# Performance work log

Hardware: AMD Instinct MI355X
Metric: run time of the kernel (lower is better)

## Reference

```python
import jax, jax.numpy as jnp
import numpy as np

STYLE_DIM = 512
NUM_DOMAINS = 8
BATCH = 16384
N_DEC_LAYERS = 4
N_EXP_LAYERS = 4   # each expert: Linear+ReLU x3, then Linear


def setup_inputs() -> dict:
    key = jax.random.key(0)
    ks = jax.random.split(key, 6)
    D, E, B = STYLE_DIM, NUM_DOMAINS, BATCH
    scale = 1.0 / np.sqrt(D)  # ~ torch Linear default init scale
    s = jax.random.normal(ks[0], (B, D), dtype=jnp.float32)
    y = jax.random.randint(ks[1], (B,), 0, E, dtype=jnp.int32)
    # decomposer params: stacked [L, out, in] / [L, out]
    dec_W = jax.random.uniform(ks[2], (N_DEC_LAYERS, D, D), jnp.float32, -scale, scale)
    dec_b = jax.random.uniform(ks[3], (N_DEC_LAYERS, D), jnp.float32, -scale, scale)
    # expert params: stacked [E, L, out, in] / [E, L, out]
    exp_W = jax.random.uniform(ks[4], (E, N_EXP_LAYERS, D, D), jnp.float32, -scale, scale)
    exp_b = jax.random.uniform(ks[5], (E, N_EXP_LAYERS, D), jnp.float32, -scale, scale)
    return {"s": s, "y": y, "dec_W": dec_W, "dec_b": dec_b, "exp_W": exp_W, "exp_b": exp_b}


def reference(s, y, dec_W, dec_b, exp_W, exp_b):
    h = s
    for l in range(N_DEC_LAYERS):
        h = jax.nn.relu(jnp.einsum('bi,oi->bo', h, dec_W[l]) + dec_b[l])
    s_unrelated = h                      # [B, D]
    s_related = s - s_unrelated          # [B, D]

    # run ALL experts on every sample (faithful to original dense compute)
    x = jnp.broadcast_to(s_related[:, None, :], (s.shape[0], NUM_DOMAINS, s.shape[1]))
    for l in range(N_EXP_LAYERS):
        x = jnp.einsum('bei,eoi->beo', x, exp_W[:, l]) + exp_b[:, l]
        if l < N_EXP_LAYERS - 1:
            x = jax.nn.relu(x)
    # gather the per-sample domain output: out[idx, y]
    s_related_tilde = jnp.take_along_axis(x, y[:, None, None].astype(jnp.int32), axis=1)[:, 0, :]
    s_tilde = s_related_tilde + s_unrelated
    return s_tilde
```

## Files before the change

kernel.cpp:

```cpp
#include <hip/hip_runtime.h>
#include <stdint.h>

#define BB 16384
#define PR2 16896
#define MAXT2 264

typedef short bf16x8 __attribute__((ext_vector_type(8)));
typedef float f32x4 __attribute__((ext_vector_type(4)));
typedef unsigned short us4v __attribute__((ext_vector_type(4)));

typedef __attribute__((address_space(1))) unsigned short gus_t;
typedef __attribute__((address_space(3))) unsigned short lus_t;

__device__ __forceinline__ unsigned short f2bf(float f) {
    unsigned int u = __float_as_uint(f);
    u += 0x7fffu + ((u >> 16) & 1u);
    return (unsigned short)(u >> 16);
}
__device__ __forceinline__ float bf2f(unsigned short h) {
    return __uint_as_float(((unsigned int)h) << 16);
}

__device__ __forceinline__ void gld16(const unsigned short* g, unsigned short* l) {
    __builtin_amdgcn_global_load_lds(
        reinterpret_cast<const gus_t*>(reinterpret_cast<uintptr_t>(g)),
        reinterpret_cast<lus_t*>(reinterpret_cast<uintptr_t>(l)),
        16, 0, 0);
}

__global__ void cvt_bf16(const float* __restrict__ src, unsigned short* __restrict__ dst, int n4) {
    int stride = gridDim.x * blockDim.x;
    for (int i = blockIdx.x * blockDim.x + threadIdx.x; i < n4; i += stride) {
        f32x4 v = reinterpret_cast<const f32x4*>(src)[i];
        us4v o;
        o[0] = f2bf(v[0]); o[1] = f2bf(v[1]); o[2] = f2bf(v[2]); o[3] = f2bf(v[3]);
        reinterpret_cast<us4v*>(dst)[i] = o;
    }
}

__global__ void bucket_init(int* perm, int* counts, int* cursors, int* tile_exp) {
    int i = blockIdx.x * blockDim.x + threadIdx.x;
    if (i < PR2) perm[i] = -1;
    if (i < 8) { counts[i] = 0; cursors[i] = 0; }
    if (i < MAXT2) tile_exp[i] = 0;
}

__global__ __launch_bounds__(1024) void bucket_count(const int* __restrict__ y, int* counts) {
    __shared__ int lc[8];
    const int t = threadIdx.x;
    if (t < 8) lc[t] = 0;
    __syncthreads();
    atomicAdd(&lc[y[blockIdx.x * 1024 + t]], 1);
    __syncthreads();
    if (t < 8) atomicAdd(&counts[t], lc[t]);
}

__global__ void bucket_scan(const int* __restrict__ counts, int* starts, int* tile_exp) {
    if (threadIdx.x == 0 && blockIdx.x == 0) {
        int s = 0;
        for (int e = 0; e < 8; ++e) {
            starts[e] = s;
            int nt = (counts[e] + 63) >> 6;
            for (int t = 0; t < nt; ++t) tile_exp[(s >> 6) + t] = e;
            s += nt << 6;
        }
        starts[8] = s;
    }
}

__global__ __launch_bounds__(1024) void bucket_scatter(const int* __restrict__ y,
                                                       const int* __restrict__ starts,
                                                       int* cursors, int* perm) {
    __shared__ int lc[8];
    __shared__ int lbase[8];
    const int t = threadIdx.x;
    if (t < 8) lc[t] = 0;
    __syncthreads();
    const int i = blockIdx.x * 1024 + t;
    const int e = y[i];
    const int r = atomicAdd(&lc[e], 1);
    __syncthreads();
    if (t < 8) lbase[t] = atomicAdd(&cursors[t], lc[t]);
    __syncthreads();
    perm[starts[e] + lbase[e] + r] = i;
}

#define STAGEW(s_, b_) do {                                              \
    const unsigned short* wp_ = Wl + ((s_) >> 4) * 262144                \
                              + (((s_) & 15) << 5) + wbase;              \
    unsigned short* ld_ = ls + 32768 + ((b_) << 14) + (t << 3);          \
    gld16(wp_,          ld_);                                            \
    gld16(wp_ +  65536, ld_ +  4096);                                    \
    gld16(wp_ + 131072, ld_ +  8192);                                    \
    gld16(wp_ + 196608, ld_ + 12288);                                    \
} while (0)

template <int PHASE>
__global__ __launch_bounds__(512) void fused4(
    const float* __restrict__ sf32,
    const unsigned short* __restrict__ srelg,
    const unsigned short* __restrict__ Wb,
    const float* __restrict__ biasb,
    unsigned short* __restrict__ srel_out,
    unsigned short* __restrict__ h_out,
    const unsigned short* __restrict__ h_in,
    float* __restrict__ outf,
    const int* __restrict__ perm,
    const int* __restrict__ tile_exp,
    const int* __restrict__ starts8)
{
    __shared__ __align__(16) unsigned short ls[81920];

    const int bid = blockIdx.x;
    int tile;
    if (PHASE == 0) {
        tile = ((bid & 7) << 5) + (bid >> 3);
    } else {
        tile = (bid & 7) * 33 + (bid >> 3);
        if ((tile << 6) >= starts8[0]) return;
    }

    const unsigned short* Wl;
    const float* bl;
    if (PHASE == 0) { Wl = Wb; bl = biasb; }
    else {
        const int e = tile_exp[tile];
        Wl = Wb + ((size_t)e << 20);
        bl = biasb + (e << 11);
    }

    const int t = threadIdx.x;
    const int w = t >> 6;
    const int lane = t & 63;
    const int lr = lane & 15;
    const int kg = lane >> 4;

    const int wbase = ((t >> 2) << 9) + (((t & 3) ^ ((t >> 3) & 3)) << 3);
    const int asrc_c = (t & 56) | ((t ^ (t >> 6)) & 7);
    const int axor = lr & 7;
    int arow_e[4], bvo[4];
#pragma unroll
    for (int m = 0; m < 4; ++m) arow_e[m] = ((m << 4) + lr) << 9;
#pragma unroll
    for (int j = 0; j < 4; ++j)
        bvo[j] = (((w << 6) + (j << 4) + lr) << 5) + ((kg ^ ((lr >> 1) & 3)) << 3);

    float bball[16];
#pragma unroll
    for (int l = 0; l < 4; ++l)
#pragma unroll
        for (int j = 0; j < 4; ++j)
            bball[(l << 2) + j] = bl[(l << 9) + (w << 6) + (j << 4) + lr];
    asm volatile("s_waitcnt vmcnt(0)" ::: "memory");

    if (PHASE == 0) {
#pragma unroll
        for (int c8 = 0; c8 < 8; ++c8) {
            const int grow = (tile << 6) + (c8 << 3) + (t >> 6);
            const float* sp = sf32 + (((size_t)grow) << 9) + (asrc_c << 3);
            f32x4 v0 = *reinterpret_cast<const f32x4*>(sp);
            f32x4 v1 = *reinterpret_cast<const f32x4*>(sp + 4);
            bf16x8 o;
#pragma unroll
            for (int q = 0; q < 4; ++q) { o[q] = (short)f2bf(v0[q]); o[q + 4] = (short)f2bf(v1[q]); }
            *reinterpret_cast<bf16x8*>(&ls[(c8 << 12) + (t << 3)]) = o;
        }
        asm volatile("s_waitcnt lgkmcnt(0)" ::: "memory");
    } else {
#pragma unroll
        for (int c8 = 0; c8 < 8; ++c8) {
            int pr = perm[(tile << 6) + (c8 << 3) + (t >> 6)];
            if (pr < 0) pr = 0;
            gld16(srelg + (((size_t)pr) << 9) + (asrc_c << 3), ls + (c8 << 12) + (t << 3));
        }
    }
    STAGEW(0, 0);
    STAGEW(1, 1);

    f32x4 acc[4][4];
#pragma unroll
    for (int m = 0; m < 4; ++m)
#pragma unroll
        for (int j = 0; j < 4; ++j)
            acc[m][j] = f32x4{0.f, 0.f, 0.f, 0.f};

    int cur = 0;
    for (int s = 0; s < 64; ++s) {
        if (s < 63) asm volatile("s_waitcnt vmcnt(4)" ::: "memory");
        else        asm volatile("s_waitcnt vmcnt(0)" ::: "memory");
        __builtin_amdgcn_s_barrier();
        asm volatile("" ::: "memory");

        int nb = cur + 2; if (nb >= 3) nb -= 3;
        if (s + 2 < 64) STAGEW(s + 2, nb);

        const int st = s & 15;
        const int sb = (st >> 1) << 6;
        const int klo = ((((st & 1) << 2) | kg) ^ axor) << 3;
        const unsigned short* lW = ls + 32768 + (cur << 14);
        bf16x8 af[4], bv[4];
#pragma unroll
        for (int m = 0; m < 4; ++m)
            af[m] = *reinterpret_cast<const bf16x8*>(&ls[arow_e[m] + sb + klo]);
#pragma unroll
        for (int j = 0; j < 4; ++j)
            bv[j] = *reinterpret_cast<const bf16x8*>(&lW[bvo[j]]);
        __builtin_amdgcn_s_setprio(1);
#pragma unroll
        for (int m = 0; m < 4; ++m)
#pragma unroll
            for (int j = 0; j < 4; ++j)
                acc[m][j] = __builtin_amdgcn_mfma_f32_16x16x32_bf16(af[m], bv[j], acc[m][j], 0, 0, 0);
        __builtin_amdgcn_s_setprio(0);

        if (st == 15 && s < 63) {
            asm volatile("" ::: "memory");
            __builtin_amdgcn_s_barrier();
            asm volatile("" ::: "memory");
            const int lbb = (s >> 4) << 2;
#pragma unroll
            for (int m = 0; m < 4; ++m)
#pragma unroll
                for (int j = 0; j < 4; ++j) {
#pragma unroll
                    for (int reg = 0; reg < 4; ++reg) {
                        const int row = (m << 4) + (kg << 2) + reg;
                        const float v = fmaxf(acc[m][j][reg] + bball[lbb + j], 0.f);
                        const int swc = (w << 3) + (((j << 1) + (lr >> 3)) ^ (row & 7));
                        ls[(row << 9) + (swc << 3) + (lr & 7)] = f2bf(v);
                    }
                    acc[m][j] = f32x4{0.f, 0.f, 0.f, 0.f};
                }
            asm volatile("s_waitcnt lgkmcnt(0)" ::: "memory");
            __builtin_amdgcn_s_barrier();
            asm volatile("" ::: "memory");
        }
        cur = cur + 1 < 3 ? cur + 1 : 0;
    }

    if (PHASE == 0) {
        asm volatile("" ::: "memory");
        __syncthreads();
#pragma unroll
        for (int m = 0; m < 4; ++m)
#pragma unroll
            for (int j = 0; j < 4; ++j)
#pragma unroll
                for (int reg = 0; reg < 4; ++reg) {
                    const int row = (m << 4) + (kg << 2) + reg;
                    const int col = (w << 6) + (j << 4) + lr;
                    const float h = fmaxf(acc[m][j][reg] + bball[12 + j], 0.f);
                    const float sv = sf32[(((size_t)((tile << 6) + row)) << 9) + col];
                    const int swc = (w << 3) + (((j << 1) + (lr >> 3)) ^ (row & 7));
                    const int idx = (row << 9) + (swc << 3) + (lr & 7);
                    ls[idx] = f2bf(sv - h);
                    ls[32768 + idx] = f2bf(h);
                }
        __syncthreads();
#pragma unroll
        for (int c8 = 0; c8 < 8; ++c8) {
            const int row = (c8 << 3) + (t >> 6);
            const size_t go = (((size_t)((tile << 6) + row)) << 9) + (asrc_c << 3);
            bf16x8 va = *reinterpret_cast<const bf16x8*>(&ls[(c8 << 12) + (t << 3)]);
            bf16x8 vh = *reinterpret_cast<const bf16x8*>(&ls[32768 + (c8 << 12) + (t << 3)]);
            *reinterpret_cast<bf16x8*>(&srel_out[go]) = va;
            *reinterpret_cast<bf16x8*>(&h_out[go]) = vh;
        }
    } else {
#pragma unroll
        for (int m = 0; m < 4; ++m) {
#pragma unroll
            for (int reg = 0; reg < 4; ++reg) {
                const int row = (m << 4) + (kg << 2) + reg;
                const int pr = perm[(tile << 6) + row];
                if (pr >= 0) {
#pragma unroll
                    for (int j = 0; j < 4; ++j) {
                        const int col = (w << 6) + (j << 4) + lr;
                        const size_t gi = (((size_t)pr) << 9) + col;
                        outf[gi] = acc[m][j][reg] + bball[12 + j] + bf2f(h_in[gi]);
                    }
                }
            }
        }
    }
}

extern "C" void kernel_launch(void* const* d_in, const int* in_sizes, int n_in,
                              void* d_out, int out_size, void* d_ws, size_t ws_size,
                              hipStream_t stream)
{
    const float* s     = (const float*)d_in[0];
    const int*   y     = (const int*)d_in[1];
    const float* dec_W = (const float*)d_in[2];
    const float* dec_b = (const float*)d_in[3];
    const float* exp_W = (const float*)d_in[4];
    const float* exp_b = (const float*)d_in[5];
    float* out = (float*)d_out;

    unsigned short* decWb = (unsigned short*)d_ws;
    unsigned short* expWb = decWb + 4 * 512 * 512;
    unsigned short* srel  = expWb + 8 * 4 * 512 * 512;
    unsigned short* hbuf  = srel + (size_t)BB * 512;
    int* perm     = (int*)(hbuf + (size_t)BB * 512);
    int* counts   = perm + PR2;
    int* cursors  = counts + 8;
    int* starts   = cursors + 8;
    int* tile_exp = starts + 9;

    cvt_bf16<<<256, 256, 0, stream>>>(dec_W, decWb, (4 * 512 * 512) / 4);
    cvt_bf16<<<2048, 256, 0, stream>>>(exp_W, expWb, (8 * 4 * 512 * 512) / 4);

    bucket_init<<<(PR2 + 255) / 256, 256, 0, stream>>>(perm, counts, cursors, tile_exp);
    bucket_count<<<BB / 1024, 1024, 0, stream>>>(y, counts);
    bucket_scan<<<1, 64, 0, stream>>>(counts, starts, tile_exp);
    bucket_scatter<<<BB / 1024, 1024, 0, stream>>>(y, starts, cursors, perm);

    fused4<0><<<256, 512, 0, stream>>>(s, nullptr, decWb, dec_b, srel, hbuf,
                                       nullptr, nullptr, nullptr, nullptr, nullptr);
    fused4<1><<<MAXT2, 512, 0, stream>>>(nullptr, srel, expWb, exp_b, nullptr, nullptr,
                                         hbuf, out, perm, tile_exp, starts + 8);
}
```

Before: 192.0 us.

## Load weight fragments directly from global into registers, shrink LDS for two blocks/CU

Weight tiles are no longer staged through LDS with async global-to-LDS copies and a triple buffer. Each lane now loads its B fragments straight from global memory into registers, using a three-deep register prefetch per layer. LDS drops to the activation tile only (64 KB), and launch bounds request two blocks per CU to raise occupancy. The cost is uncoalesced, per-lane 16-byte weight reads hitting L2, with no cross-wave sharing of weights inside a block, plus extra epilogue passes to write h and s_rel out through the smaller LDS.

```diff
diff --git a/kernel.cpp b/kernel.cpp
--- a/kernel.cpp
+++ b/kernel.cpp
@@ -85,18 +85,8 @@
     perm[starts[e] + lbase[e] + r] = i;
 }
 
-#define STAGEW(s_, b_) do {                                              \
-    const unsigned short* wp_ = Wl + ((s_) >> 4) * 262144                \
-                              + (((s_) & 15) << 5) + wbase;              \
-    unsigned short* ld_ = ls + 32768 + ((b_) << 14) + (t << 3);          \
-    gld16(wp_,          ld_);                                            \
-    gld16(wp_ +  65536, ld_ +  4096);                                    \
-    gld16(wp_ + 131072, ld_ +  8192);                                    \
-    gld16(wp_ + 196608, ld_ + 12288);                                    \
-} while (0)
-
 template <int PHASE>
-__global__ __launch_bounds__(512) void fused4(
+__global__ __launch_bounds__(512, 2) void fused4(
     const float* __restrict__ sf32,
     const unsigned short* __restrict__ srelg,
     const unsigned short* __restrict__ Wb,
@@ -109,7 +99,7 @@
     const int* __restrict__ tile_exp,
     const int* __restrict__ starts8)
 {
-    __shared__ __align__(16) unsigned short ls[81920];
+    __shared__ __align__(16) unsigned short ls[32768];
 
     const int bid = blockIdx.x;
     int tile;
@@ -135,15 +125,16 @@
     const int lr = lane & 15;
     const int kg = lane >> 4;
 
-    const int wbase = ((t >> 2) << 9) + (((t & 3) ^ ((t >> 3) & 3)) << 3);
     const int asrc_c = (t & 56) | ((t ^ (t >> 6)) & 7);
     const int axor = lr & 7;
-    int arow_e[4], bvo[4];
+    int arow_e[4];
 #pragma unroll
     for (int m = 0; m < 4; ++m) arow_e[m] = ((m << 4) + lr) << 9;
+
+    const unsigned short* wp[4];
 #pragma unroll
     for (int j = 0; j < 4; ++j)
-        bvo[j] = (((w << 6) + (j << 4) + lr) << 5) + ((kg ^ ((lr >> 1) & 3)) << 3);
+        wp[j] = Wl + (((size_t)((w << 6) + (j << 4) + lr)) << 9) + (kg << 3);
 
     float bball[16];
 #pragma unroll
@@ -151,7 +142,6 @@
 #pragma unroll
         for (int j = 0; j < 4; ++j)
             bball[(l << 2) + j] = bl[(l << 9) + (w << 6) + (j << 4) + lr];
-    asm volatile("s_waitcnt vmcnt(0)" ::: "memory");
 
     if (PHASE == 0) {
 #pragma unroll
@@ -165,7 +155,6 @@
             for (int q = 0; q < 4; ++q) { o[q] = (short)f2bf(v0[q]); o[q + 4] = (short)f2bf(v1[q]); }
             *reinterpret_cast<bf16x8*>(&ls[(c8 << 12) + (t << 3)]) = o;
         }
-        asm volatile("s_waitcnt lgkmcnt(0)" ::: "memory");
     } else {
 #pragma unroll
         for (int c8 = 0; c8 < 8; ++c8) {
@@ -173,9 +162,9 @@
             if (pr < 0) pr = 0;
             gld16(srelg + (((size_t)pr) << 9) + (asrc_c << 3), ls + (c8 << 12) + (t << 3));
         }
-    }
-    STAGEW(0, 0);
-    STAGEW(1, 1);
+        asm volatile("s_waitcnt vmcnt(0)" ::: "memory");
+    }
+    __syncthreads();
 
     f32x4 acc[4][4];
 #pragma unroll
@@ -184,40 +173,40 @@
         for (int j = 0; j < 4; ++j)
             acc[m][j] = f32x4{0.f, 0.f, 0.f, 0.f};
 
-    int cur = 0;
-    for (int s = 0; s < 64; ++s) {
-        if (s < 63) asm volatile("s_waitcnt vmcnt(4)" ::: "memory");
-        else        asm volatile("s_waitcnt vmcnt(0)" ::: "memory");
-        __builtin_amdgcn_s_barrier();
-        asm volatile("" ::: "memory");
-
-        int nb = cur + 2; if (nb >= 3) nb -= 3;
-        if (s + 2 < 64) STAGEW(s + 2, nb);
-
-        const int st = s & 15;
-        const int sb = (st >> 1) << 6;
-        const int klo = ((((st & 1) << 2) | kg) ^ axor) << 3;
-        const unsigned short* lW = ls + 32768 + (cur << 14);
-        bf16x8 af[4], bv[4];
-#pragma unroll
-        for (int m = 0; m < 4; ++m)
-            af[m] = *reinterpret_cast<const bf16x8*>(&ls[arow_e[m] + sb + klo]);
-#pragma unroll
-        for (int j = 0; j < 4; ++j)
-            bv[j] = *reinterpret_cast<const bf16x8*>(&lW[bvo[j]]);
-        __builtin_amdgcn_s_setprio(1);
-#pragma unroll
-        for (int m = 0; m < 4; ++m)
-#pragma unroll
-            for (int j = 0; j < 4; ++j)
-                acc[m][j] = __builtin_amdgcn_mfma_f32_16x16x32_bf16(af[m], bv[j], acc[m][j], 0, 0, 0);
-        __builtin_amdgcn_s_setprio(0);
-
-        if (st == 15 && s < 63) {
-            asm volatile("" ::: "memory");
-            __builtin_amdgcn_s_barrier();
-            asm volatile("" ::: "memory");
-            const int lbb = (s >> 4) << 2;
+    for (int l = 0; l < 4; ++l) {
+        const size_t lofs = ((size_t)l) << 18;
+
+        bf16x8 bv[3][4];
+#pragma unroll
+        for (int j = 0; j < 4; ++j) bv[0][j] = *reinterpret_cast<const bf16x8*>(wp[j] + lofs);
+#pragma unroll
+        for (int j = 0; j < 4; ++j) bv[1][j] = *reinterpret_cast<const bf16x8*>(wp[j] + lofs + 32);
+
+#pragma unroll
+        for (int st = 0; st < 16; ++st) {
+            const int cur = st % 3;
+            const int nxt = (st + 2) % 3;
+            if (st + 2 < 16) {
+#pragma unroll
+                for (int j = 0; j < 4; ++j)
+                    bv[nxt][j] = *reinterpret_cast<const bf16x8*>(wp[j] + lofs + (st + 2) * 32);
+            }
+            const int sb = (st >> 1) << 6;
+            const int klo = ((((st & 1) << 2) | kg) ^ axor) << 3;
+            bf16x8 af[4];
+#pragma unroll
+            for (int m = 0; m < 4; ++m)
+                af[m] = *reinterpret_cast<const bf16x8*>(&ls[arow_e[m] + sb + klo]);
+#pragma unroll
+            for (int m = 0; m < 4; ++m)
+#pragma unroll
+                for (int j = 0; j < 4; ++j)
+                    acc[m][j] = __builtin_amdgcn_mfma_f32_16x16x32_bf16(af[m], bv[cur][j], acc[m][j], 0, 0, 0);
+        }
+
+        if (l < 3) {
+            __syncthreads();
+            const int lbb = l << 2;
 #pragma unroll
             for (int m = 0; m < 4; ++m)
 #pragma unroll
@@ -231,15 +220,11 @@
                     }
                     acc[m][j] = f32x4{0.f, 0.f, 0.f, 0.f};
                 }
-            asm volatile("s_waitcnt lgkmcnt(0)" ::: "memory");
-            __builtin_amdgcn_s_barrier();
-            asm volatile("" ::: "memory");
-        }
-        cur = cur + 1 < 3 ? cur + 1 : 0;
+            __syncthreads();
+        }
     }
 
     if (PHASE == 0) {
-        asm volatile("" ::: "memory");
         __syncthreads();
 #pragma unroll
         for (int m = 0; m < 4; ++m)
@@ -252,19 +237,35 @@
                     const float h = fmaxf(acc[m][j][reg] + bball[12 + j], 0.f);
                     const float sv = sf32[(((size_t)((tile << 6) + row)) << 9) + col];
                     const int swc = (w << 3) + (((j << 1) + (lr >> 3)) ^ (row & 7));
-                    const int idx = (row << 9) + (swc << 3) + (lr & 7);
-                    ls[idx] = f2bf(sv - h);
-                    ls[32768 + idx] = f2bf(h);
+                    ls[(row << 9) + (swc << 3) + (lr & 7)] = f2bf(sv - h);
                 }
         __syncthreads();
 #pragma unroll
         for (int c8 = 0; c8 < 8; ++c8) {
             const int row = (c8 << 3) + (t >> 6);
             const size_t go = (((size_t)((tile << 6) + row)) << 9) + (asrc_c << 3);
-            bf16x8 va = *reinterpret_cast<const bf16x8*>(&ls[(c8 << 12) + (t << 3)]);
-            bf16x8 vh = *reinterpret_cast<const bf16x8*>(&ls[32768 + (c8 << 12) + (t << 3)]);
-            *reinterpret_cast<bf16x8*>(&srel_out[go]) = va;
-            *reinterpret_cast<bf16x8*>(&h_out[go]) = vh;
+            *reinterpret_cast<bf16x8*>(&srel_out[go]) =
+                *reinterpret_cast<const bf16x8*>(&ls[(c8 << 12) + (t << 3)]);
+        }
+        __syncthreads();
+#pragma unroll
+        for (int m = 0; m < 4; ++m)
+#pragma unroll
+            for (int j = 0; j < 4; ++j)
+#pragma unroll
+                for (int reg = 0; reg < 4; ++reg) {
+                    const int row = (m << 4) + (kg << 2) + reg;
+                    const float h = fmaxf(acc[m][j][reg] + bball[12 + j], 0.f);
+                    const int swc = (w << 3) + (((j << 1) + (lr >> 3)) ^ (row & 7));
+                    ls[(row << 9) + (swc << 3) + (lr & 7)] = f2bf(h);
+                }
+        __syncthreads();
+#pragma unroll
+        for (int c8 = 0; c8 < 8; ++c8) {
+            const int row = (c8 << 3) + (t >> 6);
+            const size_t go = (((size_t)((tile << 6) + row)) << 9) + (asrc_c << 3);
+            *reinterpret_cast<bf16x8*>(&h_out[go]) =
+                *reinterpret_cast<const bf16x8*>(&ls[(c8 << 12) + (t << 3)]);
         }
     } else {
 #pragma unroll
```

After: 253.5 us. 1.32x slower.

## Give each wave private weight staging slices and drop per-step block barriers

Applied to the files above, without the earlier changes.

Each wave now loads only the weight columns it consumes into its own triple-buffered LDS slice, so the per-iteration block-wide barrier in the K loop is removed and waves synchronize only on their own vmcnt. The K-step order is also rotated per tile and wave (offset) to spread global and LDS bank traffic. This trades cross-wave weight sharing for independence, so the total LDS footprint per wave changes and it relies on per-wave vmcnt being a sufficient fence for global_load_lds writes. The extra phase-1 vmcnt(0) wait after the gathered activation loads serializes the prologue a bit.

```diff
diff --git a/kernel.cpp b/kernel.cpp
--- a/kernel.cpp
+++ b/kernel.cpp
@@ -85,14 +85,14 @@
     perm[starts[e] + lbase[e] + r] = i;
 }
 
-#define STAGEW(s_, b_) do {                                              \
-    const unsigned short* wp_ = Wl + ((s_) >> 4) * 262144                \
-                              + (((s_) & 15) << 5) + wbase;              \
-    unsigned short* ld_ = ls + 32768 + ((b_) << 14) + (t << 3);          \
-    gld16(wp_,          ld_);                                            \
-    gld16(wp_ +  65536, ld_ +  4096);                                    \
-    gld16(wp_ + 131072, ld_ +  8192);                                    \
-    gld16(wp_ + 196608, ld_ + 12288);                                    \
+#define STAGE(x_) do {                                                        \
+    const unsigned short* wp_ = Wl + (((size_t)((x_) >> 4)) << 18)            \
+        + ((size_t)((((x_) & 15) + off) & 15) << 5) + wsrc_off;               \
+    unsigned short* ld_ = wdst0 + (((x_) % 3) << 11);                         \
+    gld16(wp_,         ld_);                                                  \
+    gld16(wp_ +  8192, ld_ +  512);                                           \
+    gld16(wp_ + 16384, ld_ + 1024);                                           \
+    gld16(wp_ + 24576, ld_ + 1536);                                           \
 } while (0)
 
 template <int PHASE>
@@ -134,16 +134,18 @@
     const int lane = t & 63;
     const int lr = lane & 15;
     const int kg = lane >> 4;
-
-    const int wbase = ((t >> 2) << 9) + (((t & 3) ^ ((t >> 3) & 3)) << 3);
+    const int off = ((tile * 3) + w) & 15;
+
     const int asrc_c = (t & 56) | ((t ^ (t >> 6)) & 7);
     const int axor = lr & 7;
-    int arow_e[4], bvo[4];
+    int arow_e[4];
 #pragma unroll
     for (int m = 0; m < 4; ++m) arow_e[m] = ((m << 4) + lr) << 9;
-#pragma unroll
-    for (int j = 0; j < 4; ++j)
-        bvo[j] = (((w << 6) + (j << 4) + lr) << 5) + ((kg ^ ((lr >> 1) & 3)) << 3);
+
+    const int wcb = w << 6;
+    const size_t wsrc_off = (((size_t)(wcb + (lane >> 2))) << 9) + ((lane & 3) << 3);
+    unsigned short* const wdst0 = ls + 32768 + w * 6144 + (lane << 3);
+    const int wrd0 = 32768 + w * 6144 + (lr << 5) + (kg << 3);
 
     float bball[16];
 #pragma unroll
@@ -156,7 +158,7 @@
     if (PHASE == 0) {
 #pragma unroll
         for (int c8 = 0; c8 < 8; ++c8) {
-            const int grow = (tile << 6) + (c8 << 3) + (t >> 6);
+            const int grow = (tile << 6) + (c8 << 3) + w;
             const float* sp = sf32 + (((size_t)grow) << 9) + (asrc_c << 3);
             f32x4 v0 = *reinterpret_cast<const f32x4*>(sp);
             f32x4 v1 = *reinterpret_cast<const f32x4*>(sp + 4);
@@ -169,13 +171,15 @@
     } else {
 #pragma unroll
         for (int c8 = 0; c8 < 8; ++c8) {
-            int pr = perm[(tile << 6) + (c8 << 3) + (t >> 6)];
+            int pr = perm[(tile << 6) + (c8 << 3) + w];
             if (pr < 0) pr = 0;
             gld16(srelg + (((size_t)pr) << 9) + (asrc_c << 3), ls + (c8 << 12) + (t << 3));
         }
-    }
-    STAGEW(0, 0);
-    STAGEW(1, 1);
+        asm volatile("s_waitcnt vmcnt(0)" ::: "memory");
+    }
+    STAGE(0);
+    STAGE(1);
+    __builtin_amdgcn_s_barrier();
 
     f32x4 acc[4][4];
 #pragma unroll
@@ -184,27 +188,22 @@
         for (int j = 0; j < 4; ++j)
             acc[m][j] = f32x4{0.f, 0.f, 0.f, 0.f};
 
-    int cur = 0;
     for (int s = 0; s < 64; ++s) {
         if (s < 63) asm volatile("s_waitcnt vmcnt(4)" ::: "memory");
         else        asm volatile("s_waitcnt vmcnt(0)" ::: "memory");
-        __builtin_amdgcn_s_barrier();
-        asm volatile("" ::: "memory");
-
-        int nb = cur + 2; if (nb >= 3) nb -= 3;
-        if (s + 2 < 64) STAGEW(s + 2, nb);
-
-        const int st = s & 15;
+        if (s + 2 < 64) STAGE(s + 2);
+
+        const int st = ((s & 15) + off) & 15;
         const int sb = (st >> 1) << 6;
         const int klo = ((((st & 1) << 2) | kg) ^ axor) << 3;
-        const unsigned short* lW = ls + 32768 + (cur << 14);
+        const int wb = (s % 3) << 11;
         bf16x8 af[4], bv[4];
 #pragma unroll
         for (int m = 0; m < 4; ++m)
             af[m] = *reinterpret_cast<const bf16x8*>(&ls[arow_e[m] + sb + klo]);
 #pragma unroll
         for (int j = 0; j < 4; ++j)
-            bv[j] = *reinterpret_cast<const bf16x8*>(&lW[bvo[j]]);
+            bv[j] = *reinterpret_cast<const bf16x8*>(&ls[wrd0 + wb + (j << 9)]);
         __builtin_amdgcn_s_setprio(1);
 #pragma unroll
         for (int m = 0; m < 4; ++m)
@@ -213,8 +212,7 @@
                 acc[m][j] = __builtin_amdgcn_mfma_f32_16x16x32_bf16(af[m], bv[j], acc[m][j], 0, 0, 0);
         __builtin_amdgcn_s_setprio(0);
 
-        if (st == 15 && s < 63) {
-            asm volatile("" ::: "memory");
+        if ((s & 15) == 15 && s < 63) {
             __builtin_amdgcn_s_barrier();
             asm volatile("" ::: "memory");
             const int lbb = (s >> 4) << 2;
@@ -235,11 +233,9 @@
             __builtin_amdgcn_s_barrier();
             asm volatile("" ::: "memory");
         }
-        cur = cur + 1 < 3 ? cur + 1 : 0;
     }
 
     if (PHASE == 0) {
-        asm volatile("" ::: "memory");
         __syncthreads();
 #pragma unroll
         for (int m = 0; m < 4; ++m)
@@ -259,7 +255,7 @@
         __syncthreads();
 #pragma unroll
         for (int c8 = 0; c8 < 8; ++c8) {
-            const int row = (c8 << 3) + (t >> 6);
+            const int row = (c8 << 3) + w;
             const size_t go = (((size_t)((tile << 6) + row)) << 9) + (asrc_c << 3);
             bf16x8 va = *reinterpret_cast<const bf16x8*>(&ls[(c8 << 12) + (t << 3)]);
             bf16x8 vh = *reinterpret_cast<const bf16x8*>(&ls[32768 + (c8 << 12) + (t << 3)]);
@@ -278,7 +274,7 @@
                     for (int j = 0; j < 4; ++j) {
                         const int col = (w << 6) + (j << 4) + lr;
                         const size_t gi = (((size_t)pr) << 9) + col;
-                        outf[gi] = acc[m][j][reg] + bball[12 + j] + bf2f(h_in[gi]);
+                        outf[gi] = acc[m][reg >> 2 == 0 ? j : j][reg] + bball[12 + j] + bf2f(h_in[gi]);
                     }
                 }
             }
```

After: 182.9 us. 4.8% less time.
